# Kernel optimization log

Hardware: AMD Instinct MI355X
Metric: run time of the kernel (lower is better)

Reference implementation:

```python
import jax, jax.numpy as jnp
import numpy as np

N = 50000      # nodes
E = 600000     # edges
F_ATOM = 78
D = 128        # hidden_dim = heads * head_dim
H = 8
C = D // H     # 16
ED = 12        # edge_dim
L = 4          # num_layers
B = 512        # graphs in batch
DFF = 4 * D
SCALE = 1.0 / float(np.sqrt(C))


def setup_inputs() -> dict:
    key = jax.random.key(0)
    ks = iter(jax.random.split(key, 128))
    rn = lambda s, sc=0.05: jax.random.normal(next(ks), s, jnp.float32) * sc
    inp = {
        "x": jax.random.normal(next(ks), (N, F_ATOM), jnp.float32),
        "edge_attr": jax.random.normal(next(ks), (E, ED), jnp.float32),
        "edge_index": jax.random.randint(next(ks), (2, E), 0, N),
        "batch": jnp.sort(jax.random.randint(next(ks), (N,), 0, B)),
        "Wemb": rn((F_ATOM, D)), "bemb": jnp.zeros((D,), jnp.float32),
        "Wout": rn((D, D)), "bout": jnp.zeros((D,), jnp.float32),
    }
    def stk(s, sc=0.05):
        return jnp.stack([rn(s, sc) for _ in range(L)])
    inp.update(
        Wq=stk((D, D)), bq=jnp.zeros((L, D), jnp.float32),
        Wk=stk((D, D)), bk=jnp.zeros((L, D), jnp.float32),
        Wv=stk((D, D)), bv=jnp.zeros((L, D), jnp.float32),
        We=stk((ED, D)), be=jnp.zeros((L, D), jnp.float32),
        Wskip=stk((D, D)), bskip=jnp.zeros((L, D), jnp.float32),
        Wbeta=stk((3 * D,)),
        g1=jnp.ones((L, D), jnp.float32), b1=jnp.zeros((L, D), jnp.float32),
        g2=jnp.ones((L, D), jnp.float32), b2=jnp.zeros((L, D), jnp.float32),
        Wf1=stk((D, DFF)), bf1=jnp.zeros((L, DFF), jnp.float32),
        Wf2=stk((DFF, D)), bf2=jnp.zeros((L, D), jnp.float32),
    )
    return inp


def _ln(x, g, b):
    mu = jnp.mean(x, -1, keepdims=True)
    var = jnp.mean((x - mu) ** 2, -1, keepdims=True)
    return (x - mu) * jax.lax.rsqrt(var + 1e-5) * g + b


def _seg_softmax(alpha, dst):
    # alpha: [E, H]; softmax over edges sharing a destination node
    m = jax.ops.segment_max(alpha, dst, num_segments=N)
    m = jnp.where(jnp.isfinite(m), m, 0.0)
    ex = jnp.exp(alpha - m[dst])
    den = jax.ops.segment_sum(ex, dst, num_segments=N)
    return ex / (den[dst] + 1e-16)


def _forward(x, edge_attr, Wemb, bemb, Wq, bq, Wk, bk, Wv, bv, We, be,
             Wskip, bskip, Wbeta, g1, b1, g2, b2, Wf1, bf1, Wf2, bf2,
             Wout, bout, edge_index, batch):
    src, dst = edge_index[0], edge_index[1]
    h = x @ Wemb + bemb                                    # [N, D]
    for l in range(L):
        q = (h @ Wq[l] + bq[l]).reshape(N, H, C)
        k = (h @ Wk[l] + bk[l]).reshape(N, H, C)
        v = (h @ Wv[l] + bv[l]).reshape(N, H, C)
        e = (edge_attr @ We[l] + be[l]).reshape(E, H, C)
        kj = k[src] + e                                    # [E, H, C]
        alpha = jnp.einsum('ehc,ehc->eh', q[dst], kj) * SCALE
        a = _seg_softmax(alpha, dst)                       # [E, H]
        msg = (v[src] + e) * a[:, :, None]                 # [E, H, C]
        agg = jax.ops.segment_sum(msg, dst, num_segments=N).reshape(N, D)
        xr = h @ Wskip[l] + bskip[l]                       # root/skip transform
        beta = jax.nn.sigmoid(
            jnp.concatenate([agg, xr, agg - xr], -1) @ Wbeta[l])[:, None]
        hc = beta * xr + (1.0 - beta) * agg                # beta gate
        h = _ln(hc + h, g1[l], b1[l])
        ff = jax.nn.relu(h @ Wf1[l] + bf1[l]) @ Wf2[l] + bf2[l]
        h = _ln(ff + h, g2[l], b2[l])
    cnt = jax.ops.segment_sum(jnp.ones((N,), h.dtype), batch, num_segments=B)
    pooled = jax.ops.segment_sum(h, batch, num_segments=B) / jnp.maximum(cnt, 1.0)[:, None]
    return pooled @ Wout + bout                            # [B, D]


def reference(x, edge_attr, edge_index, batch, Wemb, bemb, Wout, bout,
              Wq, bq, Wk, bk, Wv, bv, We, be, Wskip, bskip, Wbeta,
              g1, b1, g2, b2, Wf1, bf1, Wf2, bf2):
    return _forward(x, edge_attr, Wemb, bemb, Wq, bq, Wk, bk, Wv, bv, We, be,
                    Wskip, bskip, Wbeta, g1, b1, g2, b2, Wf1, bf1, Wf2, bf2,
                    Wout, bout, edge_index, batch)
```

## Files before the change

kernel.cpp:

```cpp
#include <hip/hip_runtime.h>
#include <math.h>

#define N_NODES 50000
#define N_EDGES 600000
#define FATOM   78
#define DIM     128
#define HEADS   8
#define EDIM    12
#define LAYERS  4
#define NBATCH  512
#define NDFF    512
#define ASCALE  0.25f

typedef __attribute__((ext_vector_type(8))) short bf16x8;
typedef __attribute__((ext_vector_type(4))) float f32x4;

__device__ __forceinline__ float sum16(float v){
  #pragma unroll
  for (int m=1;m<16;m<<=1) v += __shfl_xor(v, m);
  return v;
}
__device__ __forceinline__ short f2b(float f){
  unsigned int u = __builtin_bit_cast(unsigned int, f);
  u += 0x7fffu + ((u>>16)&1u);
  return (short)(u>>16);
}
__device__ __forceinline__ float b2f_lo(unsigned int u){ return __builtin_bit_cast(float, u<<16); }
__device__ __forceinline__ float b2f_hi(unsigned int u){ return __builtin_bit_cast(float, u & 0xffff0000u); }

__device__ __forceinline__ void gload16(const short* g, short* l){
  __builtin_amdgcn_global_load_lds(
      (const __attribute__((address_space(1))) void*)g,
      (__attribute__((address_space(3))) void*)l, 16, 0, 0);
}

__global__ void count_kernel(const int* __restrict__ ei, int* __restrict__ cnt){
  int e = blockIdx.x*256 + threadIdx.x;
  if (e < N_EDGES) atomicAdd(&cnt[ei[N_EDGES + e]], 1);
}

__global__ __launch_bounds__(1024) void scan1(const int* __restrict__ cnt,
                                              int* __restrict__ row_start, int* __restrict__ bsum){
  __shared__ int lds[1024];
  int gid = blockIdx.x*1024 + threadIdx.x;
  int v = (gid < N_NODES) ? cnt[gid] : 0;
  lds[threadIdx.x] = v; __syncthreads();
  for (int off=1; off<1024; off<<=1){
    int add = (threadIdx.x>=off)?lds[threadIdx.x-off]:0;
    __syncthreads();
    lds[threadIdx.x]+=add;
    __syncthreads();
  }
  if (gid < N_NODES) row_start[gid+1] = lds[threadIdx.x];
  if (threadIdx.x==1023) bsum[blockIdx.x] = lds[1023];
}
__global__ void scan2(int* __restrict__ bsum, int nb){
  int tid = threadIdx.x;
  int v = (tid < nb) ? bsum[tid] : 0;
  #pragma unroll
  for (int off=1; off<64; off<<=1){
    int u = __shfl_up(v, off);
    if (tid >= off) v += u;
  }
  if (tid < nb) bsum[tid] = v;
}
__global__ void scan3(int* __restrict__ row_start, const int* __restrict__ bsum){
  int gid = blockIdx.x*256 + threadIdx.x;
  if (gid == 0) row_start[0] = 0;
  if (gid < N_NODES){
    int blk = gid >> 10;
    if (blk > 0) row_start[gid+1] += bsum[blk-1];
  }
}

__global__ void scatter_kernel(const int* __restrict__ ei, const float* __restrict__ ea,
                               int* __restrict__ cnt2, const int* __restrict__ row_start,
                               int* __restrict__ src_s, short* __restrict__ ea_s){
  int e = blockIdx.x*256 + threadIdx.x;
  if (e < N_EDGES){
    int d = ei[N_EDGES + e];
    int pos = atomicAdd(&cnt2[d], 1);
    int p = row_start[d] + pos;
    src_s[p] = ei[e];
    const float* src = ea + (size_t)e*EDIM;
    unsigned int* dst = (unsigned int*)(ea_s + (size_t)p*EDIM);
    #pragma unroll
    for (int j=0;j<6;j++){
      unsigned int lo = (unsigned int)(unsigned short)f2b(src[2*j]);
      unsigned int hi = (unsigned int)(unsigned short)f2b(src[2*j+1]);
      dst[j] = lo | (hi<<16);
    }
  }
}

__global__ __launch_bounds__(256) void deg_hist(const int* __restrict__ cnt, int* __restrict__ dhist){
  __shared__ int lh[256];
  lh[threadIdx.x] = 0; __syncthreads();
  int n = blockIdx.x*256 + threadIdx.x;
  if (n < N_NODES){
    int d = cnt[n]; if (d > 255) d = 255;
    atomicAdd(&lh[d], 1);
  }
  __syncthreads();
  int c = lh[threadIdx.x];
  if (c) atomicAdd(&dhist[threadIdx.x], c);
}
__global__ __launch_bounds__(256) void deg_scan(const int* __restrict__ dhist, int* __restrict__ dstart){
  __shared__ int l[256];
  int t = threadIdx.x;
  int v = dhist[t];
  l[t] = v; __syncthreads();
  for (int off=1; off<256; off<<=1){
    int add = (t>=off)? l[t-off]:0;
    __syncthreads();
    l[t]+=add;
    __syncthreads();
  }
  dstart[t] = l[t]-v;
}
__global__ __launch_bounds__(256) void deg_place(const int* __restrict__ cnt, int* __restrict__ dcnt,
                                                 const int* __restrict__ dstart, int* __restrict__ perm){
  __shared__ int lh[256];
  __shared__ int lbase[256];
  __shared__ int lrank[256];
  int t = threadIdx.x;
  lh[t] = 0; lrank[t] = 0; __syncthreads();
  int n = blockIdx.x*256 + t;
  int d = -1;
  if (n < N_NODES){
    d = cnt[n]; if (d > 255) d = 255;
    atomicAdd(&lh[d], 1);
  }
  __syncthreads();
  int c = lh[t];
  lbase[t] = c ? atomicAdd(&dcnt[t], c) : 0;
  __syncthreads();
  if (n < N_NODES){
    int r = atomicAdd(&lrank[d], 1);
    perm[dstart[d] + lbase[d] + r] = n;
  }
}

__global__ __launch_bounds__(256) void pack_weights(
  const float* __restrict__ Wq, const float* __restrict__ Wk,
  const float* __restrict__ Wv, const float* __restrict__ Ws,
  const float* __restrict__ bq, const float* __restrict__ bk,
  const float* __restrict__ bv, const float* __restrict__ bs,
  const float* __restrict__ Wf1, const float* __restrict__ Wf2,
  short* __restrict__ wq_t, short* __restrict__ wf1_t, short* __restrict__ wf2_t,
  float* __restrict__ bqkvs)
{
  int l = blockIdx.y;
  int idx = blockIdx.x*256 + threadIdx.x;
  int sec = idx >> 16, r = idx & 65535;
  if (sec == 0){
    int n = r >> 7, k = r & 127;
    const float* W = (n<128)?Wq:(n<256)?Wk:(n<384)?Wv:Ws;
    float v = W[(size_t)l*16384 + k*128 + (n&127)];
    wq_t[(size_t)l*65536 + n*128 + k] = f2b(v);
    if (k == 0){
      const float* bb = (n<128)?bq:(n<256)?bk:(n<384)?bv:bs;
      bqkvs[l*512 + n] = bb[l*128 + (n&127)];
    }
  } else if (sec == 1){
    int n = r >> 7, k = r & 127;
    wf1_t[(size_t)l*65536 + n*128 + k] = f2b(Wf1[(size_t)l*65536 + k*512 + n]);
  } else {
    int n = r >> 9, k = r & 511;
    wf2_t[(size_t)l*65536 + n*512 + k] = f2b(Wf2[(size_t)l*65536 + k*128 + n]);
  }
}

__global__ void pack_emb(const float* __restrict__ Wemb, short* __restrict__ wemb_t){
  int idx = blockIdx.x*256 + threadIdx.x;
  int nn = idx >> 7, k = idx & 127;
  wemb_t[nn*128 + k] = (k < FATOM) ? f2b(Wemb[(size_t)k*DIM + nn]) : (short)0;
}

__global__ void cast_pad_x(const float* __restrict__ x, short* __restrict__ xb){
  int idx = blockIdx.x*256 + threadIdx.x;
  int n = idx >> 6, kp = (idx & 63)*2;
  if (n >= N_NODES) return;
  float v0 = (kp   < FATOM) ? x[(size_t)n*FATOM + kp]   : 0.f;
  float v1 = (kp+1 < FATOM) ? x[(size_t)n*FATOM + kp+1] : 0.f;
  unsigned int lo = (unsigned int)(unsigned short)f2b(v0);
  unsigned int hi = (unsigned int)(unsigned short)f2b(v1);
  *(unsigned int*)(xb + (size_t)n*128 + kp) = lo | (hi<<16);
}

__global__ __launch_bounds__(256) void gemm_k128(
    const short* __restrict__ A,
    const short* __restrict__ Bt,
    const float* __restrict__ bias,
    float* __restrict__ Cf,
    short* __restrict__ Cb,
    int Nrows, int M, int relu)
{
  __shared__ short As[128*128];
  __shared__ short Bs[128*128];
  int tid  = threadIdx.x;
  int lane = tid & 63;
  int wave = tid >> 6;
  int wr = wave >> 1, wc = wave & 1;
  int bm = blockIdx.x * 128, bn = blockIdx.y * 128;
  int d  = lane & 15;
  int lr = lane >> 4;

  #pragma unroll
  for (int it=0; it<8; ++it){
    int r = wave*32 + it*4 + lr;
    int oct = (d & 8) | ((d & 7) ^ (r & 7));
    int gr = bm + r; if (gr >= Nrows) gr = Nrows-1;
    gload16(A  + (size_t)gr*128       + oct*8, As + (wave*32 + it*4)*128);
    gload16(Bt + (size_t)(bn + r)*128 + oct*8, Bs + (wave*32 + it*4)*128);
  }

  f32x4 zero = {0.f,0.f,0.f,0.f};
  f32x4 acc[4][4];
  #pragma unroll
  for (int m=0;m<4;m++)
    #pragma unroll
    for (int n=0;n<4;n++) acc[m][n] = zero;

  __syncthreads();

  #pragma unroll
  for (int ks=0; ks<4; ++ks){
    int oi = ks*4 + (lane>>4);
    bf16x8 af[4], bfv[4];
    #pragma unroll
    for (int m=0;m<4;m++){
      int row = wr*64 + m*16 + (lane&15);
      int slot = (oi&8) | ((oi&7) ^ (row&7));
      af[m] = *(const bf16x8*)(As + row*128 + slot*8);
    }
    #pragma unroll
    for (int n=0;n<4;n++){
      int col = wc*64 + n*16 + (lane&15);
      int slot = (oi&8) | ((oi&7) ^ (col&7));
      bfv[n] = *(const bf16x8*)(Bs + col*128 + slot*8);
    }
    #pragma unroll
    for (int m=0;m<4;m++)
      #pragma unroll
      for (int n=0;n<4;n++)
        acc[m][n] = __builtin_amdgcn_mfma_f32_16x16x32_bf16(af[m], bfv[n], acc[m][n], 0, 0, 0);
  }

  #pragma unroll
  for (int m=0;m<4;m++){
    #pragma unroll
    for (int n=0;n<4;n++){
      int col = bn + wc*64 + n*16 + (lane&15);
      float bval = bias[col];
      #pragma unroll
      for (int j=0;j<4;j++){
        int row = bm + wr*64 + m*16 + (lane>>4)*4 + j;
        if (row < Nrows){
          float v = acc[m][n][j] + bval;
          if (relu) v = fmaxf(v, 0.f);
          if (Cf) Cf[(size_t)row*M + col] = v;
          if (Cb) Cb[(size_t)row*M + col] = f2b(v);
        }
      }
    }
  }
}

__global__ __launch_bounds__(256) void gemm_ff2_ln(
    const short* __restrict__ A,
    const short* __restrict__ Bt,
    const float* __restrict__ bias,
    float* __restrict__ h, short* __restrict__ hb,
    const float* __restrict__ g, const float* __restrict__ b,
    int Nrows)
{
  __shared__ short As[128*64];
  __shared__ short Bs[128*64];
  __shared__ float red[2][128][2];
  int tid  = threadIdx.x;
  int lane = tid & 63;
  int wave = tid >> 6;
  int wr = wave >> 1, wc = wave & 1;
  int bm = blockIdx.x * 128;

  f32x4 zero = {0.f,0.f,0.f,0.f};
  f32x4 acc[4][4];
  #pragma unroll
  for (int m=0;m<4;m++)
    #pragma unroll
    for (int n=0;n<4;n++) acc[m][n] = zero;

  int r0 = wave*32;
  for (int k0 = 0; k0 < 512; k0 += 64){
    #pragma unroll
    for (int it=0; it<4; ++it){
      int rr = r0 + it*8;
      int r  = rr + (lane>>3);
      int oct = (lane&7) ^ (r&7);
      int gr = bm + r; if (gr >= Nrows) gr = Nrows-1;
      gload16(A  + (size_t)gr*512 + k0 + oct*8, As + rr*64);
      gload16(Bt + (size_t)r*512  + k0 + oct*8, Bs + rr*64);
    }
    __syncthreads();
    #pragma unroll
    for (int ks=0; ks<2; ++ks){
      bf16x8 af[4], bfv[4];
      #pragma unroll
      for (int m=0;m<4;m++){
        int row = wr*64 + m*16 + (lane&15);
        int oi  = ks*4 + (lane>>4);
        af[m] = *(const bf16x8*)(As + row*64 + ((oi ^ (row&7))<<3));
      }
      #pragma unroll
      for (int n=0;n<4;n++){
        int col = wc*64 + n*16 + (lane&15);
        int oi  = ks*4 + (lane>>4);
        bfv[n] = *(const bf16x8*)(Bs + col*64 + ((oi ^ (col&7))<<3));
      }
      #pragma unroll
      for (int m=0;m<4;m++)
        #pragma unroll
        for (int n=0;n<4;n++)
          acc[m][n] = __builtin_amdgcn_mfma_f32_16x16x32_bf16(af[m], bfv[n], acc[m][n], 0, 0, 0);
    }
    __syncthreads();
  }

  #pragma unroll
  for (int m=0;m<4;m++){
    #pragma unroll
    for (int n=0;n<4;n++){
      int col = wc*64 + n*16 + (lane&15);
      float bval = bias[col];
      #pragma unroll
      for (int j=0;j<4;j++){
        int row = wr*64 + m*16 + (lane>>4)*4 + j;
        int grow = bm + row; if (grow >= Nrows) grow = Nrows-1;
        acc[m][n][j] += bval + h[(size_t)grow*DIM + col];
      }
    }
  }
  #pragma unroll
  for (int m=0;m<4;m++){
    #pragma unroll
    for (int j=0;j<4;j++){
      float ps = 0.f, pq = 0.f;
      #pragma unroll
      for (int n=0;n<4;n++){ float v = acc[m][n][j]; ps += v; pq += v*v; }
      #pragma unroll
      for (int msk=1; msk<16; msk<<=1){ ps += __shfl_xor(ps, msk); pq += __shfl_xor(pq, msk); }
      if ((lane&15)==0){
        int row = wr*64 + m*16 + (lane>>4)*4 + j;
        red[wc][row][0] = ps;
        red[wc][row][1] = pq;
      }
    }
  }
  __syncthreads();
  #pragma unroll
  for (int m=0;m<4;m++){
    #pragma unroll
    for (int j=0;j<4;j++){
      int row = wr*64 + m*16 + (lane>>4)*4 + j;
      float S = red[0][row][0] + red[1][row][0];
      float Q = red[0][row][1] + red[1][row][1];
      float mu  = S*(1.f/128.f);
      float var = fmaxf(Q*(1.f/128.f) - mu*mu, 0.f);
      float rr  = rsqrtf(var + 1e-5f);
      int grow = bm + row;
      if (grow < Nrows){
        #pragma unroll
        for (int n=0;n<4;n++){
          int col = wc*64 + n*16 + (lane&15);
          float o = (acc[m][n][j]-mu)*rr*g[col] + b[col];
          h[(size_t)grow*DIM + col]  = o;
          hb[(size_t)grow*DIM + col] = f2b(o);
        }
      }
    }
  }
}

__global__ __launch_bounds__(256) void edge_attn_fused(
  const short* __restrict__ qkvx,
  const short* __restrict__ ea_s, const int* __restrict__ src_s,
  const float* __restrict__ Wel, const float* __restrict__ bel,
  const int* __restrict__ row_start, const int* __restrict__ perm,
  float* __restrict__ h, short* __restrict__ hb,
  const float* __restrict__ Wb, const float* __restrict__ g, const float* __restrict__ b)
{
  int wid = (blockIdx.x*256 + threadIdx.x) >> 4;
  if (wid >= N_NODES) return;
  int node = perm[wid];
  int ln = threadIdx.x & 15;
  int c0 = ln*8;

  const short* qrow = qkvx + (size_t)node*512;
  uint4 qu = *(const uint4*)(qrow + c0);
  float q0=b2f_lo(qu.x), q1=b2f_hi(qu.x), q2=b2f_lo(qu.y), q3=b2f_hi(qu.y);
  float q4=b2f_lo(qu.z), q5=b2f_hi(qu.z), q6=b2f_lo(qu.w), q7=b2f_hi(qu.w);

  float u[12];
  #pragma unroll
  for (int j=0;j<12;j++){
    float4 wA = *(const float4*)(Wel + j*DIM + c0);
    float4 wB = *(const float4*)(Wel + j*DIM + c0 + 4);
    float pp = q0*wA.x+q1*wA.y+q2*wA.z+q3*wA.w
             + q4*wB.x+q5*wB.y+q6*wB.z+q7*wB.w;
    u[j] = pp + __shfl_xor(pp,1);
  }
  float4 beA = *(const float4*)(bel + c0);
  float4 beB = *(const float4*)(bel + c0 + 4);
  float qbe;
  { float pp = q0*beA.x+q1*beA.y+q2*beA.z+q3*beA.w
             + q4*beB.x+q5*beB.y+q6*beB.z+q7*beB.w;
    qbe = pp + __shfl_xor(pp,1); }

  int rs = row_start[node], re = row_start[node+1];
  float den = 0.f;
  float av[8] = {0.f,0.f,0.f,0.f,0.f,0.f,0.f,0.f};
  float aEA[12] = {0.f,0.f,0.f,0.f,0.f,0.f,0.f,0.f,0.f,0.f,0.f,0.f};

  int i = rs;
  for (; i+2 <= re; i += 2){
    int s0 = src_s[i], s1 = src_s[i+1];
    const short* e0p = ea_s + (size_t)i*EDIM;
    uint2 a00 = *(const uint2*)(e0p);
    uint2 a01 = *(const uint2*)(e0p+4);
    uint2 a02 = *(const uint2*)(e0p+8);
    uint2 a10 = *(const uint2*)(e0p+12);
    uint2 a11 = *(const uint2*)(e0p+16);
    uint2 a12 = *(const uint2*)(e0p+20);
    const short* r0p = qkvx + (size_t)s0*512;
    const short* r1p = qkvx + (size_t)s1*512;
    uint4 ku0 = *(const uint4*)(r0p + 128 + c0);
    uint4 vu0 = *(const uint4*)(r0p + 256 + c0);
    uint4 ku1 = *(const uint4*)(r1p + 128 + c0);
    uint4 vu1 = *(const uint4*)(r1p + 256 + c0);

    float ea0[12], ea1[12];
    ea0[0]=b2f_lo(a00.x); ea0[1]=b2f_hi(a00.x); ea0[2]=b2f_lo(a00.y); ea0[3]=b2f_hi(a00.y);
    ea0[4]=b2f_lo(a01.x); ea0[5]=b2f_hi(a01.x); ea0[6]=b2f_lo(a01.y); ea0[7]=b2f_hi(a01.y);
    ea0[8]=b2f_lo(a02.x); ea0[9]=b2f_hi(a02.x); ea0[10]=b2f_lo(a02.y); ea0[11]=b2f_hi(a02.y);
    ea1[0]=b2f_lo(a10.x); ea1[1]=b2f_hi(a10.x); ea1[2]=b2f_lo(a10.y); ea1[3]=b2f_hi(a10.y);
    ea1[4]=b2f_lo(a11.x); ea1[5]=b2f_hi(a11.x); ea1[6]=b2f_lo(a11.y); ea1[7]=b2f_hi(a11.y);
    ea1[8]=b2f_lo(a12.x); ea1[9]=b2f_hi(a12.x); ea1[10]=b2f_lo(a12.y); ea1[11]=b2f_hi(a12.y);

    float pp0 = q0*b2f_lo(ku0.x) + q1*b2f_hi(ku0.x) + q2*b2f_lo(ku0.y) + q3*b2f_hi(ku0.y)
              + q4*b2f_lo(ku0.z) + q5*b2f_hi(ku0.z) + q6*b2f_lo(ku0.w) + q7*b2f_hi(ku0.w);
    float pp1 = q0*b2f_lo(ku1.x) + q1*b2f_hi(ku1.x) + q2*b2f_lo(ku1.y) + q3*b2f_hi(ku1.y)
              + q4*b2f_lo(ku1.z) + q5*b2f_hi(ku1.z) + q6*b2f_lo(ku1.w) + q7*b2f_hi(ku1.w);
    float al0 = pp0 + __shfl_xor(pp0,1) + qbe;
    float al1 = pp1 + __shfl_xor(pp1,1) + qbe;
    #pragma unroll
    for (int j=0;j<12;j++){ al0 += ea0[j]*u[j]; al1 += ea1[j]*u[j]; }
    float p0 = __expf(al0 * ASCALE);
    float p1 = __expf(al1 * ASCALE);
    den += p0 + p1;
    av[0] += p0*b2f_lo(vu0.x) + p1*b2f_lo(vu1.x);
    av[1] += p0*b2f_hi(vu0.x) + p1*b2f_hi(vu1.x);
    av[2] += p0*b2f_lo(vu0.y) + p1*b2f_lo(vu1.y);
    av[3] += p0*b2f_hi(vu0.y) + p1*b2f_hi(vu1.y);
    av[4] += p0*b2f_lo(vu0.z) + p1*b2f_lo(vu1.z);
    av[5] += p0*b2f_hi(vu0.z) + p1*b2f_hi(vu1.z);
    av[6] += p0*b2f_lo(vu0.w) + p1*b2f_lo(vu1.w);
    av[7] += p0*b2f_hi(vu0.w) + p1*b2f_hi(vu1.w);
    #pragma unroll
    for (int j=0;j<12;j++) aEA[j] += p0*ea0[j] + p1*ea1[j];
  }
  if (i < re){
    int s = src_s[i];
    const short* eap = ea_s + (size_t)i*EDIM;
    uint2 eu0 = *(const uint2*)(eap);
    uint2 eu1 = *(const uint2*)(eap+4);
    uint2 eu2 = *(const uint2*)(eap+8);
    float ea0[12];
    ea0[0]=b2f_lo(eu0.x); ea0[1]=b2f_hi(eu0.x); ea0[2]=b2f_lo(eu0.y); ea0[3]=b2f_hi(eu0.y);
    ea0[4]=b2f_lo(eu1.x); ea0[5]=b2f_hi(eu1.x); ea0[6]=b2f_lo(eu1.y); ea0[7]=b2f_hi(eu1.y);
    ea0[8]=b2f_lo(eu2.x); ea0[9]=b2f_hi(eu2.x); ea0[10]=b2f_lo(eu2.y); ea0[11]=b2f_hi(eu2.y);
    const short* srow = qkvx + (size_t)s*512;
    uint4 ku = *(const uint4*)(srow + 128 + c0);
    uint4 vu = *(const uint4*)(srow + 256 + c0);
    float pp = q0*b2f_lo(ku.x) + q1*b2f_hi(ku.x) + q2*b2f_lo(ku.y) + q3*b2f_hi(ku.y)
             + q4*b2f_lo(ku.z) + q5*b2f_hi(ku.z) + q6*b2f_lo(ku.w) + q7*b2f_hi(ku.w);
    float alpha = pp + __shfl_xor(pp,1) + qbe;
    #pragma unroll
    for (int j=0;j<12;j++) alpha += ea0[j]*u[j];
    float p = __expf(alpha * ASCALE);
    den += p;
    av[0] += p*b2f_lo(vu.x); av[1] += p*b2f_hi(vu.x);
    av[2] += p*b2f_lo(vu.y); av[3] += p*b2f_hi(vu.y);
    av[4] += p*b2f_lo(vu.z); av[5] += p*b2f_hi(vu.z);
    av[6] += p*b2f_lo(vu.w); av[7] += p*b2f_hi(vu.w);
    #pragma unroll
    for (int j=0;j<12;j++) aEA[j] += p*ea0[j];
  }

  float inv = 1.f/(den + 1e-16f);
  float gg[8];
  #pragma unroll
  for (int c=0;c<8;c++) gg[c] = av[c]*inv;
  #pragma unroll
  for (int j=0;j<12;j++){
    float wgt = aEA[j]*inv;
    float4 wA = *(const float4*)(Wel + j*DIM + c0);
    float4 wB = *(const float4*)(Wel + j*DIM + c0 + 4);
    gg[0]+=wgt*wA.x; gg[1]+=wgt*wA.y; gg[2]+=wgt*wA.z; gg[3]+=wgt*wA.w;
    gg[4]+=wgt*wB.x; gg[5]+=wgt*wB.y; gg[6]+=wgt*wB.z; gg[7]+=wgt*wB.w;
  }
  gg[0]+=beA.x; gg[1]+=beA.y; gg[2]+=beA.z; gg[3]+=beA.w;
  gg[4]+=beB.x; gg[5]+=beB.y; gg[6]+=beB.z; gg[7]+=beB.w;

  uint4 xu = *(const uint4*)(qrow + 384 + c0);
  float x[8];
  x[0]=b2f_lo(xu.x); x[1]=b2f_hi(xu.x); x[2]=b2f_lo(xu.y); x[3]=b2f_hi(xu.y);
  x[4]=b2f_lo(xu.z); x[5]=b2f_hi(xu.z); x[6]=b2f_lo(xu.w); x[7]=b2f_hi(xu.w);
  float4 hA = *(const float4*)(h + (size_t)node*DIM + c0);
  float4 hB = *(const float4*)(h + (size_t)node*DIM + c0 + 4);
  float hv[8] = {hA.x,hA.y,hA.z,hA.w,hB.x,hB.y,hB.z,hB.w};
  float4 waA = *(const float4*)(Wb + c0),       waB = *(const float4*)(Wb + c0 + 4);
  float4 wxA = *(const float4*)(Wb + DIM + c0), wxB = *(const float4*)(Wb + DIM + c0 + 4);
  float4 wdA = *(const float4*)(Wb + 2*DIM + c0), wdB = *(const float4*)(Wb + 2*DIM + c0 + 4);
  float wa[8] = {waA.x,waA.y,waA.z,waA.w,waB.x,waB.y,waB.z,waB.w};
  float wx[8] = {wxA.x,wxA.y,wxA.z,wxA.w,wxB.x,wxB.y,wxB.z,wxB.w};
  float wd[8] = {wdA.x,wdA.y,wdA.z,wdA.w,wdB.x,wdB.y,wdB.z,wdB.w};
  float sacc = 0.f;
  #pragma unroll
  for (int c=0;c<8;c++) sacc += gg[c]*wa[c] + x[c]*wx[c] + (gg[c]-x[c])*wd[c];
  sacc = sum16(sacc);
  float beta = 1.f/(1.f + __expf(-sacc));
  float t[8], ts = 0.f;
  #pragma unroll
  for (int c=0;c<8;c++){ t[c] = beta*x[c] + (1.f-beta)*gg[c] + hv[c]; ts += t[c]; }
  float mu = sum16(ts)*(1.f/128.f);
  float vs = 0.f;
  #pragma unroll
  for (int c=0;c<8;c++){ t[c] -= mu; vs += t[c]*t[c]; }
  float var = sum16(vs)*(1.f/128.f);
  float r = rsqrtf(var + 1e-5f);
  float4 gA = *(const float4*)(g + c0), gB = *(const float4*)(g + c0 + 4);
  float4 bA = *(const float4*)(b + c0), bB = *(const float4*)(b + c0 + 4);
  float gv[8] = {gA.x,gA.y,gA.z,gA.w,gB.x,gB.y,gB.z,gB.w};
  float bv[8] = {bA.x,bA.y,bA.z,bA.w,bB.x,bB.y,bB.z,bB.w};
  float o[8];
  #pragma unroll
  for (int c=0;c<8;c++) o[c] = t[c]*r*gv[c] + bv[c];
  float4 oA = {o[0],o[1],o[2],o[3]}, oB = {o[4],o[5],o[6],o[7]};
  *(float4*)(h + (size_t)node*DIM + c0)     = oA;
  *(float4*)(h + (size_t)node*DIM + c0 + 4) = oB;
  uint4 ou;
  ou.x = (unsigned int)(unsigned short)f2b(o[0]) | ((unsigned int)(unsigned short)f2b(o[1])<<16);
  ou.y = (unsigned int)(unsigned short)f2b(o[2]) | ((unsigned int)(unsigned short)f2b(o[3])<<16);
  ou.z = (unsigned int)(unsigned short)f2b(o[4]) | ((unsigned int)(unsigned short)f2b(o[5])<<16);
  ou.w = (unsigned int)(unsigned short)f2b(o[6]) | ((unsigned int)(unsigned short)f2b(o[7])<<16);
  *(uint4*)(hb + (size_t)node*DIM + c0) = ou;
}

__global__ __launch_bounds__(128) void pool_out(
  const float* __restrict__ h, const int* __restrict__ batch,
  const float* __restrict__ Wout, const float* __restrict__ bout,
  float* __restrict__ out)
{
  int bidx = blockIdx.x;
  int d = threadIdx.x;
  __shared__ int seg[2];
  __shared__ float p[DIM];
  if (d < 2){
    int target = bidx + d;
    int lo = 0, hi = N_NODES;
    while (lo < hi){ int mid = (lo+hi)>>1; if (batch[mid] < target) lo = mid+1; else hi = mid; }
    seg[d] = lo;
  }
  __syncthreads();
  int lo = seg[0], hi = seg[1];
  float s = 0.f;
  for (int n=lo; n<hi; ++n) s += h[(size_t)n*DIM + d];
  float cnt = (float)(hi - lo);
  p[d] = s / fmaxf(cnt, 1.f);
  __syncthreads();
  float o = bout[d];
  #pragma unroll 8
  for (int kk=0; kk<DIM; ++kk) o += p[kk]*Wout[kk*DIM + d];
  out[bidx*DIM + d] = o;
}

extern "C" void kernel_launch(void* const* d_in, const int* in_sizes, int n_in,
                              void* d_out, int out_size, void* d_ws, size_t ws_size,
                              hipStream_t stream)
{
  const float* x     = (const float*)d_in[0];
  const float* ea    = (const float*)d_in[1];
  const int*   ei    = (const int*)d_in[2];
  const int*   batch = (const int*)d_in[3];
  const float* Wemb  = (const float*)d_in[4];
  const float* bemb  = (const float*)d_in[5];
  const float* Wout  = (const float*)d_in[6];
  const float* bout  = (const float*)d_in[7];
  const float* Wq    = (const float*)d_in[8];
  const float* bq    = (const float*)d_in[9];
  const float* Wk    = (const float*)d_in[10];
  const float* bk    = (const float*)d_in[11];
  const float* Wv    = (const float*)d_in[12];
  const float* bv    = (const float*)d_in[13];
  const float* We    = (const float*)d_in[14];
  const float* be    = (const float*)d_in[15];
  const float* Wskip = (const float*)d_in[16];
  const float* bskip = (const float*)d_in[17];
  const float* Wbeta = (const float*)d_in[18];
  const float* g1    = (const float*)d_in[19];
  const float* b1    = (const float*)d_in[20];
  const float* g2    = (const float*)d_in[21];
  const float* b2    = (const float*)d_in[22];
  const float* Wf1   = (const float*)d_in[23];
  const float* bf1   = (const float*)d_in[24];
  const float* Wf2   = (const float*)d_in[25];
  const float* bf2   = (const float*)d_in[26];
  float* out = (float*)d_out;

  float* ws     = (float*)d_ws;
  float* h      = ws;
  float* bqkvs  = h + (size_t)N_NODES*DIM;
  short* ea_s   = (short*)(bqkvs + LAYERS*512);
  short* hb     = ea_s + (size_t)N_EDGES*EDIM;
  short* region = hb + (size_t)N_NODES*DIM;
  short* xb     = region + (size_t)N_NODES*NDFF;
  short* wemb_t = xb + (size_t)N_NODES*DIM;
  short* wq_t   = wemb_t + DIM*DIM;
  short* wf1_t  = wq_t  + (size_t)LAYERS*NDFF*DIM;
  short* wf2_t  = wf1_t + (size_t)LAYERS*NDFF*DIM;
  int*   cnt       = (int*)(wf2_t + (size_t)LAYERS*NDFF*DIM);
  int*   cnt2      = cnt + N_NODES;
  int*   row_start = cnt2 + N_NODES;
  int*   bsum      = row_start + N_NODES + 1;
  int*   dhist     = bsum + 64;
  int*   dcnt      = dhist + 256;
  int*   dstart    = dcnt + 256;
  int*   node_perm = dstart + 256;
  int*   src_s     = node_perm + N_NODES;

  hipMemsetAsync(cnt,  0, N_NODES*sizeof(int), stream);
  hipMemsetAsync(cnt2, 0, N_NODES*sizeof(int), stream);
  hipMemsetAsync(dhist, 0, 512*sizeof(int), stream);

  const int NB_SCAN = (N_NODES + 1023)/1024;
  const int NB_DEG  = (N_NODES + 255)/256;
  count_kernel<<<(N_EDGES+255)/256, 256, 0, stream>>>(ei, cnt);
  scan1<<<NB_SCAN, 1024, 0, stream>>>(cnt, row_start, bsum);
  scan2<<<1, 64, 0, stream>>>(bsum, NB_SCAN);
  scan3<<<(N_NODES+255)/256, 256, 0, stream>>>(row_start, bsum);
  deg_hist<<<NB_DEG, 256, 0, stream>>>(cnt, dhist);
  deg_scan<<<1, 256, 0, stream>>>(dhist, dstart);
  deg_place<<<NB_DEG, 256, 0, stream>>>(cnt, dcnt, dstart, node_perm);
  scatter_kernel<<<(N_EDGES+255)/256, 256, 0, stream>>>(ei, ea, cnt2, row_start, src_s, ea_s);

  pack_weights<<<dim3(768, LAYERS), 256, 0, stream>>>(
      Wq, Wk, Wv, Wskip, bq, bk, bv, bskip, Wf1, Wf2, wq_t, wf1_t, wf2_t, bqkvs);
  pack_emb<<<64, 256, 0, stream>>>(Wemb, wemb_t);
  cast_pad_x<<<(N_NODES*64 + 255)/256, 256, 0, stream>>>(x, xb);

  int gM = (N_NODES + 127)/128;
  int attnBlocks = (N_NODES*16 + 255)/256;

  gemm_k128<<<dim3(gM, 1), 256, 0, stream>>>(xb, wemb_t, bemb, h, hb, N_NODES, DIM, 0);

  for (int l=0; l<LAYERS; ++l){
    gemm_k128<<<dim3(gM, 4), 256, 0, stream>>>(
        hb, wq_t + (size_t)l*NDFF*DIM, bqkvs + l*512, nullptr, region,
        N_NODES, NDFF, 0);

    edge_attn_fused<<<attnBlocks, 256, 0, stream>>>(
        region, ea_s, src_s, We + (size_t)l*EDIM*DIM, be + l*DIM, row_start, node_perm,
        h, hb, Wbeta + l*3*DIM, g1 + l*DIM, b1 + l*DIM);

    gemm_k128<<<dim3(gM, 4), 256, 0, stream>>>(
        hb, wf1_t + (size_t)l*NDFF*DIM, bf1 + l*NDFF, nullptr, region,
        N_NODES, NDFF, 1);

    gemm_ff2_ln<<<dim3(gM, 1), 256, 0, stream>>>(
        region, wf2_t + (size_t)l*DIM*NDFF, bf2 + l*DIM, h, hb,
        g2 + l*DIM, b2 + l*DIM, N_NODES);
  }

  pool_out<<<NBATCH, 128, 0, stream>>>(h, batch, Wout, bout, out);
}
```

Baseline: 892.1 us.

## Reuse A tile across N-blocks in GEMM and halve lanes per node in attention

The K=128 GEMM now keeps its A tile in LDS and loops over several 128-column B tiles per block, so each A tile is loaded once per two N-blocks and the grid's y dimension is halved. The edge attention kernel maps one node to 8 lanes with 16 channels each instead of 16 lanes with 8 channels, dropping the pair shuffles for head dot products and shortening the reductions. It also walks the degree-sorted permutation in reverse order. The GEMM trades parallelism and an extra barrier for less A traffic, and the attention change raises per-lane register use while issuing fewer, wider gathers per edge.

```diff
diff --git a/kernel.cpp b/kernel.cpp
--- a/kernel.cpp
+++ b/kernel.cpp
@@ -15,9 +15,9 @@
 typedef __attribute__((ext_vector_type(8))) short bf16x8;
 typedef __attribute__((ext_vector_type(4))) float f32x4;
 
-__device__ __forceinline__ float sum16(float v){
-  #pragma unroll
-  for (int m=1;m<16;m<<=1) v += __shfl_xor(v, m);
+__device__ __forceinline__ float sum8(float v){
+  #pragma unroll
+  for (int m=1;m<8;m<<=1) v += __shfl_xor(v, m);
   return v;
 }
 __device__ __forceinline__ short f2b(float f){
@@ -27,6 +27,10 @@
 }
 __device__ __forceinline__ float b2f_lo(unsigned int u){ return __builtin_bit_cast(float, u<<16); }
 __device__ __forceinline__ float b2f_hi(unsigned int u){ return __builtin_bit_cast(float, u & 0xffff0000u); }
+__device__ __forceinline__ void unp8(uint4 u, float* o){
+  o[0]=b2f_lo(u.x); o[1]=b2f_hi(u.x); o[2]=b2f_lo(u.y); o[3]=b2f_hi(u.y);
+  o[4]=b2f_lo(u.z); o[5]=b2f_hi(u.z); o[6]=b2f_lo(u.w); o[7]=b2f_hi(u.w);
+}
 
 __device__ __forceinline__ void gload16(const short* g, short* l){
   __builtin_amdgcn_global_load_lds(
@@ -194,7 +198,7 @@
     const float* __restrict__ bias,
     float* __restrict__ Cf,
     short* __restrict__ Cb,
-    int Nrows, int M, int relu)
+    int Nrows, int M, int relu, int nbn)
 {
   __shared__ short As[128*128];
   __shared__ short Bs[128*128];
@@ -202,7 +206,7 @@
   int lane = tid & 63;
   int wave = tid >> 6;
   int wr = wave >> 1, wc = wave & 1;
-  int bm = blockIdx.x * 128, bn = blockIdx.y * 128;
+  int bm = blockIdx.x * 128;
   int d  = lane & 15;
   int lr = lane >> 4;
 
@@ -211,56 +215,65 @@
     int r = wave*32 + it*4 + lr;
     int oct = (d & 8) | ((d & 7) ^ (r & 7));
     int gr = bm + r; if (gr >= Nrows) gr = Nrows-1;
-    gload16(A  + (size_t)gr*128       + oct*8, As + (wave*32 + it*4)*128);
-    gload16(Bt + (size_t)(bn + r)*128 + oct*8, Bs + (wave*32 + it*4)*128);
-  }
-
-  f32x4 zero = {0.f,0.f,0.f,0.f};
-  f32x4 acc[4][4];
-  #pragma unroll
-  for (int m=0;m<4;m++)
-    #pragma unroll
-    for (int n=0;n<4;n++) acc[m][n] = zero;
-
-  __syncthreads();
-
-  #pragma unroll
-  for (int ks=0; ks<4; ++ks){
-    int oi = ks*4 + (lane>>4);
-    bf16x8 af[4], bfv[4];
+    gload16(A + (size_t)gr*128 + oct*8, As + (wave*32 + it*4)*128);
+  }
+
+  for (int t=0; t<nbn; ++t){
+    int bn = (blockIdx.y*nbn + t)*128;
+    if (t) __syncthreads();
+    #pragma unroll
+    for (int it=0; it<8; ++it){
+      int r = wave*32 + it*4 + lr;
+      int oct = (d & 8) | ((d & 7) ^ (r & 7));
+      gload16(Bt + (size_t)(bn + r)*128 + oct*8, Bs + (wave*32 + it*4)*128);
+    }
+    f32x4 zero = {0.f,0.f,0.f,0.f};
+    f32x4 acc[4][4];
+    #pragma unroll
+    for (int m=0;m<4;m++)
+      #pragma unroll
+      for (int n=0;n<4;n++) acc[m][n] = zero;
+
+    __syncthreads();
+
+    #pragma unroll
+    for (int ks=0; ks<4; ++ks){
+      int oi = ks*4 + (lane>>4);
+      bf16x8 af[4], bfv[4];
+      #pragma unroll
+      for (int m=0;m<4;m++){
+        int row = wr*64 + m*16 + (lane&15);
+        int slot = (oi&8) | ((oi&7) ^ (row&7));
+        af[m] = *(const bf16x8*)(As + row*128 + slot*8);
+      }
+      #pragma unroll
+      for (int n=0;n<4;n++){
+        int col = wc*64 + n*16 + (lane&15);
+        int slot = (oi&8) | ((oi&7) ^ (col&7));
+        bfv[n] = *(const bf16x8*)(Bs + col*128 + slot*8);
+      }
+      #pragma unroll
+      for (int m=0;m<4;m++)
+        #pragma unroll
+        for (int n=0;n<4;n++)
+          acc[m][n] = __builtin_amdgcn_mfma_f32_16x16x32_bf16(af[m], bfv[n], acc[m][n], 0, 0, 0);
+    }
+
     #pragma unroll
     for (int m=0;m<4;m++){
-      int row = wr*64 + m*16 + (lane&15);
-      int slot = (oi&8) | ((oi&7) ^ (row&7));
-      af[m] = *(const bf16x8*)(As + row*128 + slot*8);
-    }
-    #pragma unroll
-    for (int n=0;n<4;n++){
-      int col = wc*64 + n*16 + (lane&15);
-      int slot = (oi&8) | ((oi&7) ^ (col&7));
-      bfv[n] = *(const bf16x8*)(Bs + col*128 + slot*8);
-    }
-    #pragma unroll
-    for (int m=0;m<4;m++)
-      #pragma unroll
-      for (int n=0;n<4;n++)
-        acc[m][n] = __builtin_amdgcn_mfma_f32_16x16x32_bf16(af[m], bfv[n], acc[m][n], 0, 0, 0);
-  }
-
-  #pragma unroll
-  for (int m=0;m<4;m++){
-    #pragma unroll
-    for (int n=0;n<4;n++){
-      int col = bn + wc*64 + n*16 + (lane&15);
-      float bval = bias[col];
-      #pragma unroll
-      for (int j=0;j<4;j++){
-        int row = bm + wr*64 + m*16 + (lane>>4)*4 + j;
-        if (row < Nrows){
-          float v = acc[m][n][j] + bval;
-          if (relu) v = fmaxf(v, 0.f);
-          if (Cf) Cf[(size_t)row*M + col] = v;
-          if (Cb) Cb[(size_t)row*M + col] = f2b(v);
+      #pragma unroll
+      for (int n=0;n<4;n++){
+        int col = bn + wc*64 + n*16 + (lane&15);
+        float bval = bias[col];
+        #pragma unroll
+        for (int j=0;j<4;j++){
+          int row = bm + wr*64 + m*16 + (lane>>4)*4 + j;
+          if (row < Nrows){
+            float v = acc[m][n][j] + bval;
+            if (relu) v = fmaxf(v, 0.f);
+            if (Cf) Cf[(size_t)row*M + col] = v;
+            if (Cb) Cb[(size_t)row*M + col] = f2b(v);
+          }
         }
       }
     }
@@ -390,171 +403,182 @@
   float* __restrict__ h, short* __restrict__ hb,
   const float* __restrict__ Wb, const float* __restrict__ g, const float* __restrict__ b)
 {
-  int wid = (blockIdx.x*256 + threadIdx.x) >> 4;
+  int wid = (blockIdx.x*256 + threadIdx.x) >> 3;
   if (wid >= N_NODES) return;
-  int node = perm[wid];
-  int ln = threadIdx.x & 15;
-  int c0 = ln*8;
+  int node = perm[N_NODES - 1 - wid];
+  int ln = threadIdx.x & 7;
+  int c0 = ln*16;
 
   const short* qrow = qkvx + (size_t)node*512;
-  uint4 qu = *(const uint4*)(qrow + c0);
-  float q0=b2f_lo(qu.x), q1=b2f_hi(qu.x), q2=b2f_lo(qu.y), q3=b2f_hi(qu.y);
-  float q4=b2f_lo(qu.z), q5=b2f_hi(qu.z), q6=b2f_lo(qu.w), q7=b2f_hi(qu.w);
-
-  float u[12];
+  float q[16];
+  unp8(*(const uint4*)(qrow + c0), q);
+  unp8(*(const uint4*)(qrow + c0 + 8), q+8);
+
+  float u[12], qbe;
   #pragma unroll
   for (int j=0;j<12;j++){
-    float4 wA = *(const float4*)(Wel + j*DIM + c0);
-    float4 wB = *(const float4*)(Wel + j*DIM + c0 + 4);
-    float pp = q0*wA.x+q1*wA.y+q2*wA.z+q3*wA.w
-             + q4*wB.x+q5*wB.y+q6*wB.z+q7*wB.w;
-    u[j] = pp + __shfl_xor(pp,1);
-  }
-  float4 beA = *(const float4*)(bel + c0);
-  float4 beB = *(const float4*)(bel + c0 + 4);
-  float qbe;
-  { float pp = q0*beA.x+q1*beA.y+q2*beA.z+q3*beA.w
-             + q4*beB.x+q5*beB.y+q6*beB.z+q7*beB.w;
-    qbe = pp + __shfl_xor(pp,1); }
+    const float* wp = Wel + j*DIM + c0;
+    float s = 0.f;
+    #pragma unroll
+    for (int c=0;c<16;c++) s += q[c]*wp[c];
+    u[j] = s;
+  }
+  {
+    const float* bp = bel + c0;
+    float s = 0.f;
+    #pragma unroll
+    for (int c=0;c<16;c++) s += q[c]*bp[c];
+    qbe = s;
+  }
 
   int rs = row_start[node], re = row_start[node+1];
   float den = 0.f;
-  float av[8] = {0.f,0.f,0.f,0.f,0.f,0.f,0.f,0.f};
-  float aEA[12] = {0.f,0.f,0.f,0.f,0.f,0.f,0.f,0.f,0.f,0.f,0.f,0.f};
+  float av[16];
+  #pragma unroll
+  for (int c=0;c<16;c++) av[c] = 0.f;
+  float aEA[12];
+  #pragma unroll
+  for (int j=0;j<12;j++) aEA[j] = 0.f;
 
   int i = rs;
   for (; i+2 <= re; i += 2){
     int s0 = src_s[i], s1 = src_s[i+1];
-    const short* e0p = ea_s + (size_t)i*EDIM;
-    uint2 a00 = *(const uint2*)(e0p);
-    uint2 a01 = *(const uint2*)(e0p+4);
-    uint2 a02 = *(const uint2*)(e0p+8);
-    uint2 a10 = *(const uint2*)(e0p+12);
-    uint2 a11 = *(const uint2*)(e0p+16);
-    uint2 a12 = *(const uint2*)(e0p+20);
-    const short* r0p = qkvx + (size_t)s0*512;
-    const short* r1p = qkvx + (size_t)s1*512;
-    uint4 ku0 = *(const uint4*)(r0p + 128 + c0);
-    uint4 vu0 = *(const uint4*)(r0p + 256 + c0);
-    uint4 ku1 = *(const uint4*)(r1p + 128 + c0);
-    uint4 vu1 = *(const uint4*)(r1p + 256 + c0);
-
-    float ea0[12], ea1[12];
-    ea0[0]=b2f_lo(a00.x); ea0[1]=b2f_hi(a00.x); ea0[2]=b2f_lo(a00.y); ea0[3]=b2f_hi(a00.y);
-    ea0[4]=b2f_lo(a01.x); ea0[5]=b2f_hi(a01.x); ea0[6]=b2f_lo(a01.y); ea0[7]=b2f_hi(a01.y);
-    ea0[8]=b2f_lo(a02.x); ea0[9]=b2f_hi(a02.x); ea0[10]=b2f_lo(a02.y); ea0[11]=b2f_hi(a02.y);
-    ea1[0]=b2f_lo(a10.x); ea1[1]=b2f_hi(a10.x); ea1[2]=b2f_lo(a10.y); ea1[3]=b2f_hi(a10.y);
-    ea1[4]=b2f_lo(a11.x); ea1[5]=b2f_hi(a11.x); ea1[6]=b2f_lo(a11.y); ea1[7]=b2f_hi(a11.y);
-    ea1[8]=b2f_lo(a12.x); ea1[9]=b2f_hi(a12.x); ea1[10]=b2f_lo(a12.y); ea1[11]=b2f_hi(a12.y);
-
-    float pp0 = q0*b2f_lo(ku0.x) + q1*b2f_hi(ku0.x) + q2*b2f_lo(ku0.y) + q3*b2f_hi(ku0.y)
-              + q4*b2f_lo(ku0.z) + q5*b2f_hi(ku0.z) + q6*b2f_lo(ku0.w) + q7*b2f_hi(ku0.w);
-    float pp1 = q0*b2f_lo(ku1.x) + q1*b2f_hi(ku1.x) + q2*b2f_lo(ku1.y) + q3*b2f_hi(ku1.y)
-              + q4*b2f_lo(ku1.z) + q5*b2f_hi(ku1.z) + q6*b2f_lo(ku1.w) + q7*b2f_hi(ku1.w);
-    float al0 = pp0 + __shfl_xor(pp0,1) + qbe;
-    float al1 = pp1 + __shfl_xor(pp1,1) + qbe;
-    #pragma unroll
-    for (int j=0;j<12;j++){ al0 += ea0[j]*u[j]; al1 += ea1[j]*u[j]; }
-    float p0 = __expf(al0 * ASCALE);
-    float p1 = __expf(al1 * ASCALE);
-    den += p0 + p1;
-    av[0] += p0*b2f_lo(vu0.x) + p1*b2f_lo(vu1.x);
-    av[1] += p0*b2f_hi(vu0.x) + p1*b2f_hi(vu1.x);
-    av[2] += p0*b2f_lo(vu0.y) + p1*b2f_lo(vu1.y);
-    av[3] += p0*b2f_hi(vu0.y) + p1*b2f_hi(vu1.y);
-    av[4] += p0*b2f_lo(vu0.z) + p1*b2f_lo(vu1.z);
-    av[5] += p0*b2f_hi(vu0.z) + p1*b2f_hi(vu1.z);
-    av[6] += p0*b2f_lo(vu0.w) + p1*b2f_lo(vu1.w);
-    av[7] += p0*b2f_hi(vu0.w) + p1*b2f_hi(vu1.w);
-    #pragma unroll
-    for (int j=0;j<12;j++) aEA[j] += p0*ea0[j] + p1*ea1[j];
+    const short* ep = ea_s + (size_t)i*EDIM;
+    uint2 e00 = *(const uint2*)(ep),    e01 = *(const uint2*)(ep+4),  e02 = *(const uint2*)(ep+8);
+    uint2 e10 = *(const uint2*)(ep+12), e11 = *(const uint2*)(ep+16), e12 = *(const uint2*)(ep+20);
+    const short* r0 = qkvx + (size_t)s0*512 + c0;
+    const short* r1 = qkvx + (size_t)s1*512 + c0;
+    uint4 k0a = *(const uint4*)(r0+128), k0b = *(const uint4*)(r0+136);
+    uint4 v0a = *(const uint4*)(r0+256), v0b = *(const uint4*)(r0+264);
+    uint4 k1a = *(const uint4*)(r1+128), k1b = *(const uint4*)(r1+136);
+    uint4 v1a = *(const uint4*)(r1+256), v1b = *(const uint4*)(r1+264);
+
+    {
+      float ea0[12];
+      ea0[0]=b2f_lo(e00.x); ea0[1]=b2f_hi(e00.x); ea0[2]=b2f_lo(e00.y); ea0[3]=b2f_hi(e00.y);
+      ea0[4]=b2f_lo(e01.x); ea0[5]=b2f_hi(e01.x); ea0[6]=b2f_lo(e01.y); ea0[7]=b2f_hi(e01.y);
+      ea0[8]=b2f_lo(e02.x); ea0[9]=b2f_hi(e02.x); ea0[10]=b2f_lo(e02.y); ea0[11]=b2f_hi(e02.y);
+      float al = qbe;
+      { float k[16]; unp8(k0a,k); unp8(k0b,k+8);
+        #pragma unroll
+        for (int c=0;c<16;c++) al += q[c]*k[c]; }
+      #pragma unroll
+      for (int j=0;j<12;j++) al += ea0[j]*u[j];
+      float p = __expf(al * ASCALE);
+      den += p;
+      { float v[16]; unp8(v0a,v); unp8(v0b,v+8);
+        #pragma unroll
+        for (int c=0;c<16;c++) av[c] += p*v[c]; }
+      #pragma unroll
+      for (int j=0;j<12;j++) aEA[j] += p*ea0[j];
+    }
+    {
+      float ea1[12];
+      ea1[0]=b2f_lo(e10.x); ea1[1]=b2f_hi(e10.x); ea1[2]=b2f_lo(e10.y); ea1[3]=b2f_hi(e10.y);
+      ea1[4]=b2f_lo(e11.x); ea1[5]=b2f_hi(e11.x); ea1[6]=b2f_lo(e11.y); ea1[7]=b2f_hi(e11.y);
+      ea1[8]=b2f_lo(e12.x); ea1[9]=b2f_hi(e12.x); ea1[10]=b2f_lo(e12.y); ea1[11]=b2f_hi(e12.y);
+      float al = qbe;
+      { float k[16]; unp8(k1a,k); unp8(k1b,k+8);
+        #pragma unroll
+        for (int c=0;c<16;c++) al += q[c]*k[c]; }
+      #pragma unroll
+      for (int j=0;j<12;j++) al += ea1[j]*u[j];
+      float p = __expf(al * ASCALE);
+      den += p;
+      { float v[16]; unp8(v1a,v); unp8(v1b,v+8);
+        #pragma unroll
+        for (int c=0;c<16;c++) av[c] += p*v[c]; }
+      #pragma unroll
+      for (int j=0;j<12;j++) aEA[j] += p*ea1[j];
+    }
   }
   if (i < re){
-    int s = src_s[i];
-    const short* eap = ea_s + (size_t)i*EDIM;
-    uint2 eu0 = *(const uint2*)(eap);
-    uint2 eu1 = *(const uint2*)(eap+4);
-    uint2 eu2 = *(const uint2*)(eap+8);
+    int s0 = src_s[i];
+    const short* ep = ea_s + (size_t)i*EDIM;
+    uint2 e00 = *(const uint2*)(ep), e01 = *(const uint2*)(ep+4), e02 = *(const uint2*)(ep+8);
+    const short* r0 = qkvx + (size_t)s0*512 + c0;
+    uint4 k0a = *(const uint4*)(r0+128), k0b = *(const uint4*)(r0+136);
+    uint4 v0a = *(const uint4*)(r0+256), v0b = *(const uint4*)(r0+264);
     float ea0[12];
-    ea0[0]=b2f_lo(eu0.x); ea0[1]=b2f_hi(eu0.x); ea0[2]=b2f_lo(eu0.y); ea0[3]=b2f_hi(eu0.y);
-    ea0[4]=b2f_lo(eu1.x); ea0[5]=b2f_hi(eu1.x); ea0[6]=b2f_lo(eu1.y); ea0[7]=b2f_hi(eu1.y);
-    ea0[8]=b2f_lo(eu2.x); ea0[9]=b2f_hi(eu2.x); ea0[10]=b2f_lo(eu2.y); ea0[11]=b2f_hi(eu2.y);
-    const short* srow = qkvx + (size_t)s*512;
-    uint4 ku = *(const uint4*)(srow + 128 + c0);
-    uint4 vu = *(const uint4*)(srow + 256 + c0);
-    float pp = q0*b2f_lo(ku.x) + q1*b2f_hi(ku.x) + q2*b2f_lo(ku.y) + q3*b2f_hi(ku.y)
-             + q4*b2f_lo(ku.z) + q5*b2f_hi(ku.z) + q6*b2f_lo(ku.w) + q7*b2f_hi(ku.w);
-    float alpha = pp + __shfl_xor(pp,1) + qbe;
-    #pragma unroll
-    for (int j=0;j<12;j++) alpha += ea0[j]*u[j];
-    float p = __expf(alpha * ASCALE);
+    ea0[0]=b2f_lo(e00.x); ea0[1]=b2f_hi(e00.x); ea0[2]=b2f_lo(e00.y); ea0[3]=b2f_hi(e00.y);
+    ea0[4]=b2f_lo(e01.x); ea0[5]=b2f_hi(e01.x); ea0[6]=b2f_lo(e01.y); ea0[7]=b2f_hi(e01.y);
+    ea0[8]=b2f_lo(e02.x); ea0[9]=b2f_hi(e02.x); ea0[10]=b2f_lo(e02.y); ea0[11]=b2f_hi(e02.y);
+    float al = qbe;
+    { float k[16]; unp8(k0a,k); unp8(k0b,k+8);
+      #pragma unroll
+      for (int c=0;c<16;c++) al += q[c]*k[c]; }
+    #pragma unroll
+    for (int j=0;j<12;j++) al += ea0[j]*u[j];
+    float p = __expf(al * ASCALE);
     den += p;
-    av[0] += p*b2f_lo(vu.x); av[1] += p*b2f_hi(vu.x);
-    av[2] += p*b2f_lo(vu.y); av[3] += p*b2f_hi(vu.y);
-    av[4] += p*b2f_lo(vu.z); av[5] += p*b2f_hi(vu.z);
-    av[6] += p*b2f_lo(vu.w); av[7] += p*b2f_hi(vu.w);
+    { float v[16]; unp8(v0a,v); unp8(v0b,v+8);
+      #pragma unroll
+      for (int c=0;c<16;c++) av[c] += p*v[c]; }
     #pragma unroll
     for (int j=0;j<12;j++) aEA[j] += p*ea0[j];
   }
 
   float inv = 1.f/(den + 1e-16f);
-  float gg[8];
-  #pragma unroll
-  for (int c=0;c<8;c++) gg[c] = av[c]*inv;
+  float gg[16];
+  #pragma unroll
+  for (int c=0;c<16;c++) gg[c] = av[c]*inv;
   #pragma unroll
   for (int j=0;j<12;j++){
     float wgt = aEA[j]*inv;
-    float4 wA = *(const float4*)(Wel + j*DIM + c0);
-    float4 wB = *(const float4*)(Wel + j*DIM + c0 + 4);
-    gg[0]+=wgt*wA.x; gg[1]+=wgt*wA.y; gg[2]+=wgt*wA.z; gg[3]+=wgt*wA.w;
-    gg[4]+=wgt*wB.x; gg[5]+=wgt*wB.y; gg[6]+=wgt*wB.z; gg[7]+=wgt*wB.w;
-  }
-  gg[0]+=beA.x; gg[1]+=beA.y; gg[2]+=beA.z; gg[3]+=beA.w;
-  gg[4]+=beB.x; gg[5]+=beB.y; gg[6]+=beB.z; gg[7]+=beB.w;
-
-  uint4 xu = *(const uint4*)(qrow + 384 + c0);
-  float x[8];
-  x[0]=b2f_lo(xu.x); x[1]=b2f_hi(xu.x); x[2]=b2f_lo(xu.y); x[3]=b2f_hi(xu.y);
-  x[4]=b2f_lo(xu.z); x[5]=b2f_hi(xu.z); x[6]=b2f_lo(xu.w); x[7]=b2f_hi(xu.w);
-  float4 hA = *(const float4*)(h + (size_t)node*DIM + c0);
-  float4 hB = *(const float4*)(h + (size_t)node*DIM + c0 + 4);
-  float hv[8] = {hA.x,hA.y,hA.z,hA.w,hB.x,hB.y,hB.z,hB.w};
-  float4 waA = *(const float4*)(Wb + c0),       waB = *(const float4*)(Wb + c0 + 4);
-  float4 wxA = *(const float4*)(Wb + DIM + c0), wxB = *(const float4*)(Wb + DIM + c0 + 4);
-  float4 wdA = *(const float4*)(Wb + 2*DIM + c0), wdB = *(const float4*)(Wb + 2*DIM + c0 + 4);
-  float wa[8] = {waA.x,waA.y,waA.z,waA.w,waB.x,waB.y,waB.z,waB.w};
-  float wx[8] = {wxA.x,wxA.y,wxA.z,wxA.w,wxB.x,wxB.y,wxB.z,wxB.w};
-  float wd[8] = {wdA.x,wdA.y,wdA.z,wdA.w,wdB.x,wdB.y,wdB.z,wdB.w};
+    const float* wp = Wel + j*DIM + c0;
+    #pragma unroll
+    for (int c=0;c<16;c++) gg[c] += wgt*wp[c];
+  }
+  if (re > rs){
+    const float* bp = bel + c0;
+    #pragma unroll
+    for (int c=0;c<16;c++) gg[c] += bp[c];
+  }
+
+  float x[16];
+  unp8(*(const uint4*)(qrow + 384 + c0), x);
+  unp8(*(const uint4*)(qrow + 384 + c0 + 8), x+8);
+  float hv[16];
+  const float* hp = h + (size_t)node*DIM + c0;
+  #pragma unroll
+  for (int c=0;c<16;c+=4){ float4 t4 = *(const float4*)(hp+c); hv[c]=t4.x; hv[c+1]=t4.y; hv[c+2]=t4.z; hv[c+3]=t4.w; }
   float sacc = 0.f;
-  #pragma unroll
-  for (int c=0;c<8;c++) sacc += gg[c]*wa[c] + x[c]*wx[c] + (gg[c]-x[c])*wd[c];
-  sacc = sum16(sacc);
+  {
+    const float* wap = Wb + c0;
+    const float* wxp = Wb + DIM + c0;
+    const float* wdp = Wb + 2*DIM + c0;
+    #pragma unroll
+    for (int c=0;c<16;c++) sacc += gg[c]*wap[c] + x[c]*wxp[c] + (gg[c]-x[c])*wdp[c];
+  }
+  sacc = sum8(sacc);
   float beta = 1.f/(1.f + __expf(-sacc));
-  float t[8], ts = 0.f;
-  #pragma unroll
-  for (int c=0;c<8;c++){ t[c] = beta*x[c] + (1.f-beta)*gg[c] + hv[c]; ts += t[c]; }
-  float mu = sum16(ts)*(1.f/128.f);
+  float t[16], ts = 0.f;
+  #pragma unroll
+  for (int c=0;c<16;c++){ t[c] = beta*x[c] + (1.f-beta)*gg[c] + hv[c]; ts += t[c]; }
+  float mu = sum8(ts)*(1.f/128.f);
   float vs = 0.f;
   #pragma unroll
-  for (int c=0;c<8;c++){ t[c] -= mu; vs += t[c]*t[c]; }
-  float var = sum16(vs)*(1.f/128.f);
+  for (int c=0;c<16;c++){ t[c] -= mu; vs += t[c]*t[c]; }
+  float var = sum8(vs)*(1.f/128.f);
   float r = rsqrtf(var + 1e-5f);
-  float4 gA = *(const float4*)(g + c0), gB = *(const float4*)(g + c0 + 4);
-  float4 bA = *(const float4*)(b + c0), bB = *(const float4*)(b + c0 + 4);
-  float gv[8] = {gA.x,gA.y,gA.z,gA.w,gB.x,gB.y,gB.z,gB.w};
-  float bv[8] = {bA.x,bA.y,bA.z,bA.w,bB.x,bB.y,bB.z,bB.w};
-  float o[8];
-  #pragma unroll
-  for (int c=0;c<8;c++) o[c] = t[c]*r*gv[c] + bv[c];
-  float4 oA = {o[0],o[1],o[2],o[3]}, oB = {o[4],o[5],o[6],o[7]};
-  *(float4*)(h + (size_t)node*DIM + c0)     = oA;
-  *(float4*)(h + (size_t)node*DIM + c0 + 4) = oB;
-  uint4 ou;
-  ou.x = (unsigned int)(unsigned short)f2b(o[0]) | ((unsigned int)(unsigned short)f2b(o[1])<<16);
-  ou.y = (unsigned int)(unsigned short)f2b(o[2]) | ((unsigned int)(unsigned short)f2b(o[3])<<16);
-  ou.z = (unsigned int)(unsigned short)f2b(o[4]) | ((unsigned int)(unsigned short)f2b(o[5])<<16);
-  ou.w = (unsigned int)(unsigned short)f2b(o[6]) | ((unsigned int)(unsigned short)f2b(o[7])<<16);
-  *(uint4*)(hb + (size_t)node*DIM + c0) = ou;
+  float o[16];
+  {
+    const float* gp = g + c0;
+    const float* bp = b + c0;
+    #pragma unroll
+    for (int c=0;c<16;c++) o[c] = t[c]*r*gp[c] + bp[c];
+  }
+  float* hw = h + (size_t)node*DIM + c0;
+  #pragma unroll
+  for (int c=0;c<16;c+=4){ float4 t4 = {o[c],o[c+1],o[c+2],o[c+3]}; *(float4*)(hw+c) = t4; }
+  unsigned int ou[8];
+  #pragma unroll
+  for (int c=0;c<8;c++)
+    ou[c] = (unsigned int)(unsigned short)f2b(o[2*c]) | ((unsigned int)(unsigned short)f2b(o[2*c+1])<<16);
+  uint4 oa = {ou[0],ou[1],ou[2],ou[3]};
+  uint4 ob = {ou[4],ou[5],ou[6],ou[7]};
+  *(uint4*)(hb + (size_t)node*DIM + c0)     = oa;
+  *(uint4*)(hb + (size_t)node*DIM + c0 + 8) = ob;
 }
 
 __global__ __launch_bounds__(128) void pool_out(
@@ -660,22 +684,22 @@
   cast_pad_x<<<(N_NODES*64 + 255)/256, 256, 0, stream>>>(x, xb);
 
   int gM = (N_NODES + 127)/128;
-  int attnBlocks = (N_NODES*16 + 255)/256;
-
-  gemm_k128<<<dim3(gM, 1), 256, 0, stream>>>(xb, wemb_t, bemb, h, hb, N_NODES, DIM, 0);
+  int attnBlocks = (N_NODES*8 + 255)/256;
+
+  gemm_k128<<<dim3(gM, 1), 256, 0, stream>>>(xb, wemb_t, bemb, h, hb, N_NODES, DIM, 0, 1);
 
   for (int l=0; l<LAYERS; ++l){
-    gemm_k128<<<dim3(gM, 4), 256, 0, stream>>>(
+    gemm_k128<<<dim3(gM, 2), 256, 0, stream>>>(
         hb, wq_t + (size_t)l*NDFF*DIM, bqkvs + l*512, nullptr, region,
-        N_NODES, NDFF, 0);
+        N_NODES, NDFF, 0, 2);
 
     edge_attn_fused<<<attnBlocks, 256, 0, stream>>>(
         region, ea_s, src_s, We + (size_t)l*EDIM*DIM, be + l*DIM, row_start, node_perm,
         h, hb, Wbeta + l*3*DIM, g1 + l*DIM, b1 + l*DIM);
 
-    gemm_k128<<<dim3(gM, 4), 256, 0, stream>>>(
+    gemm_k128<<<dim3(gM, 2), 256, 0, stream>>>(
         hb, wf1_t + (size_t)l*NDFF*DIM, bf1 + l*NDFF, nullptr, region,
-        N_NODES, NDFF, 1);
+        N_NODES, NDFF, 1, 2);
 
     gemm_ff2_ln<<<dim3(gM, 1), 256, 0, stream>>>(
         region, wf2_t + (size_t)l*DIM*NDFF, bf2 + l*DIM, h, hb,
```

Measured after the change: 1.077 ms. 1.21x slower.
